# Optimization experiments

Measured on AMD Instinct MI355X. Metric: run time of the kernel, lower is better.

The kernel has to match this reference:

```python
import jax, jax.numpy as jnp
import numpy as np

EMBED = 768
HEADS = 12
HEAD_DIM = EMBED // HEADS
HIDDEN = 4 * EMBED
B, N = 8, 1024
EPS = 1e-5


def layernorm(x, g, b):
    mu = jnp.mean(x, axis=-1, keepdims=True)
    var = jnp.var(x, axis=-1, keepdims=True)
    return (x - mu) * jax.lax.rsqrt(var + EPS) * g + b


def setup_inputs() -> dict:
    key = jax.random.key(0)
    ks = jax.random.split(key, 8)
    s_qkv = 1.0 / np.sqrt(EMBED)
    s_fc1 = 1.0 / np.sqrt(EMBED)
    s_fc2 = 1.0 / np.sqrt(HIDDEN)
    return {
        "x": jax.random.normal(ks[0], (B, N, EMBED), dtype=jnp.float32),
        "ln1_g": jnp.ones((EMBED,), jnp.float32),
        "ln1_b": jnp.zeros((EMBED,), jnp.float32),
        "qkv_w": jax.random.uniform(ks[1], (3 * EMBED, EMBED), jnp.float32, -s_qkv, s_qkv),
        "qkv_b": jnp.zeros((3 * EMBED,), jnp.float32),
        "proj_w": jax.random.uniform(ks[2], (EMBED, EMBED), jnp.float32, -s_qkv, s_qkv),
        "proj_b": jnp.zeros((EMBED,), jnp.float32),
        "ln2_g": jnp.ones((EMBED,), jnp.float32),
        "ln2_b": jnp.zeros((EMBED,), jnp.float32),
        "fc1_w": jax.random.uniform(ks[3], (HIDDEN, EMBED), jnp.float32, -s_fc1, s_fc1),
        "fc1_b": jnp.zeros((HIDDEN,), jnp.float32),
        "fc2_w": jax.random.uniform(ks[4], (EMBED, HIDDEN), jnp.float32, -s_fc2, s_fc2),
        "fc2_b": jnp.zeros((EMBED,), jnp.float32),
    }


def reference(x, ln1_g, ln1_b, qkv_w, qkv_b, proj_w, proj_b,
              ln2_g, ln2_b, fc1_w, fc1_b, fc2_w, fc2_b):
    b, n, d = x.shape
    # --- attention sublayer ---
    h = layernorm(x, ln1_g, ln1_b)
    qkv = h @ qkv_w.T + qkv_b                      # [b,n,3d]
    qkv = qkv.reshape(b, n, 3, HEADS, HEAD_DIM).transpose(2, 0, 3, 1, 4)
    q, k, v = qkv[0], qkv[1], qkv[2]               # [b,h,n,hd]
    scores = jnp.einsum('bhqd,bhkd->bhqk', q, k) * (HEAD_DIM ** -0.5)
    attn = jax.nn.softmax(scores, axis=-1)
    ctx = jnp.einsum('bhqk,bhkd->bhqd', attn, v)   # [b,h,n,hd]
    ctx = ctx.transpose(0, 2, 1, 3).reshape(b, n, d)
    x = x + (ctx @ proj_w.T + proj_b)
    # --- MLP sublayer ---
    h = layernorm(x, ln2_g, ln2_b)
    h = jax.nn.gelu(h @ fc1_w.T + fc1_b, approximate=False)
    x = x + (h @ fc2_w.T + fc2_b)
    return x
```

## Files before the change

kernel.cpp:

```cpp
#include <hip/hip_runtime.h>
#include <cstdint>

typedef __bf16 bf16_t;
typedef __attribute__((ext_vector_type(8))) __bf16 bf16x8;
typedef __attribute__((ext_vector_type(4))) __bf16 bf16x4;
typedef __attribute__((ext_vector_type(4))) float f32x4;

#define MFMA16(a, b, c) __builtin_amdgcn_mfma_f32_16x16x32_bf16((a), (b), (c), 0, 0, 0)

#define GLOAD16(g, l) __builtin_amdgcn_global_load_lds(                      \
    (const __attribute__((address_space(1))) void*)(g),                      \
    (__attribute__((address_space(3))) void*)(l), 16, 0, 0)

__device__ inline float gelu_f(float v) {
    const float u = v + 0.044715f * v * v * v;
    return v / (1.0f + exp2f(-2.3022038f * u));
}

__global__ __launch_bounds__(256) void cvt4_kernel(const float* __restrict__ s0, bf16_t* __restrict__ d0,
                                                   const float* __restrict__ s1, bf16_t* __restrict__ d1,
                                                   const float* __restrict__ s2, bf16_t* __restrict__ d2,
                                                   const float* __restrict__ s3, bf16_t* __restrict__ d3) {
    const int blk = blockIdx.x;
    const float* s; bf16_t* d; int base;
    if (blk < 864)       { s = s0; d = d0; base = blk; }
    else if (blk < 1152) { s = s1; d = d1; base = blk - 864; }
    else if (blk < 2304) { s = s2; d = d2; base = blk - 1152; }
    else                 { s = s3; d = d3; base = blk - 2304; }
    const int i = (base * 256 + threadIdx.x) * 8;
    const float4* sp = (const float4*)(s + i);
    float4 a = sp[0], b = sp[1];
    bf16x8 o;
    o[0] = (bf16_t)a.x; o[1] = (bf16_t)a.y; o[2] = (bf16_t)a.z; o[3] = (bf16_t)a.w;
    o[4] = (bf16_t)b.x; o[5] = (bf16_t)b.y; o[6] = (bf16_t)b.z; o[7] = (bf16_t)b.w;
    *(bf16x8*)(d + i) = o;
}

__global__ __launch_bounds__(256) void ln_kernel(const float* __restrict__ x,
                                                 const float* __restrict__ gw,
                                                 const float* __restrict__ bw,
                                                 bf16_t* __restrict__ out) {
    const int row  = blockIdx.x * 4 + (threadIdx.x >> 6);
    const int lane = threadIdx.x & 63;
    const float4* xr = (const float4*)(x + (long)row * 768);
    float4 v[3];
    float s = 0.f, q = 0.f;
#pragma unroll
    for (int j = 0; j < 3; ++j) {
        v[j] = xr[j * 64 + lane];
        s += v[j].x + v[j].y + v[j].z + v[j].w;
        q += v[j].x * v[j].x + v[j].y * v[j].y + v[j].z * v[j].z + v[j].w * v[j].w;
    }
#pragma unroll
    for (int off = 32; off > 0; off >>= 1) {
        s += __shfl_xor(s, off);
        q += __shfl_xor(q, off);
    }
    const float mu = s * (1.0f / 768.0f);
    const float rs = rsqrtf(q * (1.0f / 768.0f) - mu * mu + 1e-5f);
#pragma unroll
    for (int j = 0; j < 3; ++j) {
        float4 g4 = ((const float4*)gw)[j * 64 + lane];
        float4 b4 = ((const float4*)bw)[j * 64 + lane];
        bf16x4 o;
        o[0] = (bf16_t)((v[j].x - mu) * rs * g4.x + b4.x);
        o[1] = (bf16_t)((v[j].y - mu) * rs * g4.y + b4.y);
        o[2] = (bf16_t)((v[j].z - mu) * rs * g4.z + b4.z);
        o[3] = (bf16_t)((v[j].w - mu) * rs * g4.w + b4.w);
        *(bf16x4*)(out + (long)row * 768 + (j * 64 + lane) * 4) = o;
    }
}

template <int MODE, int NC, int RPX>
__global__ __launch_bounds__(256) void gemm_bt(const bf16_t* __restrict__ A,
                                               const bf16_t* __restrict__ Bw,
                                               const float* __restrict__ bias,
                                               bf16_t* __restrict__ outb,
                                               bf16_t* __restrict__ o1,
                                               bf16_t* __restrict__ o2,
                                               int Nn, int K) {
    __shared__ __align__(16) bf16_t As[2][128 * 32];
    __shared__ __align__(16) bf16_t Bs[2][128 * 32];
    __shared__ __align__(16) bf16_t Ts[4 * 16 * 72];
    const int id = blockIdx.x;
    const int xcd = id & 7, sblk = id >> 3;
    const int tn = (sblk % NC) * 128;
    const int tm = (xcd * RPX + sblk / NC) * 128;
    const int w = threadIdx.x >> 6, l = threadIdx.x & 63;
    const int quad = l >> 4, r16 = l & 15;
    const int wm = (w >> 1) * 64, wn = (w & 1) * 64;
    f32x4 acc[4][4] = {};
    const bf16_t* ga = A  + (long)(tm + w * 32 + (l >> 2)) * K + (l & 3) * 8;
    const bf16_t* gb = Bw + (long)(tn + w * 32 + (l >> 2)) * K + (l & 3) * 8;
    const int lw = w * 1024;

    GLOAD16(ga,          &As[0][lw]);
    GLOAD16(ga + 16 * K, &As[0][lw + 512]);
    GLOAD16(gb,          &Bs[0][lw]);
    GLOAD16(gb + 16 * K, &Bs[0][lw + 512]);

    int cur = 0;
    for (int k0 = 0; k0 < K; k0 += 32) {
        asm volatile("s_waitcnt vmcnt(0)" ::: "memory");
        __syncthreads();
        if (k0 + 32 < K) {
            const bf16_t* gan = ga + k0 + 32;
            const bf16_t* gbn = gb + k0 + 32;
            GLOAD16(gan,          &As[cur ^ 1][lw]);
            GLOAD16(gan + 16 * K, &As[cur ^ 1][lw + 512]);
            GLOAD16(gbn,          &Bs[cur ^ 1][lw]);
            GLOAD16(gbn + 16 * K, &Bs[cur ^ 1][lw + 512]);
        }
        bf16x8 af[4], bfr[4];
#pragma unroll
        for (int i = 0; i < 4; ++i) {
            af[i]  = *(const bf16x8*)&As[cur][(wm + i * 16 + r16) * 32 + quad * 8];
            bfr[i] = *(const bf16x8*)&Bs[cur][(wn + i * 16 + r16) * 32 + quad * 8];
        }
#pragma unroll
        for (int i = 0; i < 4; ++i)
#pragma unroll
            for (int j = 0; j < 4; ++j)
                acc[i][j] = MFMA16(af[i], bfr[j], acc[i][j]);
        cur ^= 1;
    }

    bf16_t* tw = Ts + w * 16 * 72;
    if (MODE == 0) {
        const int sect = (tn + wn) / 768;
        const int cwb  = tn + wn - sect * 768;
        const int h    = cwb >> 6;
        if (sect == 2) {
#pragma unroll
            for (int i = 0; i < 4; ++i) {
                const int r0 = tm + wm + i * 16 + quad * 4;
                const int b = r0 >> 10, n0 = r0 & 1023;
#pragma unroll
                for (int j = 0; j < 4; ++j) {
                    const int d = j * 16 + r16;
                    const float bv = bias[tn + wn + j * 16 + r16];
                    bf16_t* dst = o2 + ((long)(b * 12 + h) * 64 + d) * 1024;
#pragma unroll
                    for (int rr = 0; rr < 4; ++rr) {
                        const int nn = n0 + rr;
                        const int c = ((nn & 15) << 3) | ((nn >> 4) & 7);
                        dst[(nn & 0x380) + c] = (bf16_t)(acc[i][j][rr] + bv);
                    }
                }
            }
        } else {
            bf16_t* dstbuf = (sect == 0 ? outb : o1);
#pragma unroll
            for (int i = 0; i < 4; ++i) {
#pragma unroll
                for (int j = 0; j < 4; ++j) {
                    const float bv = bias[tn + wn + j * 16 + r16];
#pragma unroll
                    for (int rr = 0; rr < 4; ++rr)
                        tw[(quad * 4 + rr) * 72 + j * 16 + r16] = (bf16_t)(acc[i][j][rr] + bv);
                }
                const int tok = tm + wm + i * 16 + (l >> 2);
                const int b = tok >> 10, n0 = tok & 1023;
                const long base = (long)(b * 12 + h) * 65536 + (long)n0 * 64;
#pragma unroll
                for (int it = 0; it < 2; ++it) {
                    bf16x8 vv = *(const bf16x8*)&tw[(l >> 2) * 72 + (l & 3) * 8 + it * 32];
                    *(bf16x8*)(dstbuf + base + (l & 3) * 8 + it * 32) = vv;
                }
            }
        }
    } else {
#pragma unroll
        for (int i = 0; i < 4; ++i) {
#pragma unroll
            for (int j = 0; j < 4; ++j) {
                const float bv = bias[tn + wn + j * 16 + r16];
#pragma unroll
                for (int rr = 0; rr < 4; ++rr)
                    tw[(quad * 4 + rr) * 72 + j * 16 + r16] = (bf16_t)gelu_f(acc[i][j][rr] + bv);
            }
            const int grow = tm + wm + i * 16 + (l >> 2);
#pragma unroll
            for (int it = 0; it < 2; ++it) {
                bf16x8 vv = *(const bf16x8*)&tw[(l >> 2) * 72 + (l & 3) * 8 + it * 32];
                *(bf16x8*)(outb + (long)grow * Nn + tn + wn + (l & 3) * 8 + it * 32) = vv;
            }
        }
    }
}

__global__ __launch_bounds__(256) void gemm_res64(const bf16_t* __restrict__ A,
                                                  const bf16_t* __restrict__ Bw,
                                                  const float* __restrict__ bias,
                                                  const float* __restrict__ res,
                                                  float* __restrict__ outf,
                                                  int Nn, int K) {
    __shared__ __align__(16) bf16_t As[2][64 * 32];
    __shared__ __align__(16) bf16_t Bs[2][128 * 32];
    __shared__ __align__(16) float  Tf[4 * 16 * 68];
    const int id = blockIdx.x;
    const int xcd = id & 7, sblk = id >> 3;
    const int tn = (sblk % 6) * 128;
    const int tm = (xcd * 16 + sblk / 6) * 64;
    const int w = threadIdx.x >> 6, l = threadIdx.x & 63;
    const int quad = l >> 4, r16 = l & 15;
    const int wm = (w >> 1) * 32, wn = (w & 1) * 64;
    f32x4 acc[2][4] = {};
    const bf16_t* ga = A  + (long)(tm + w * 16 + (l >> 2)) * K + (l & 3) * 8;
    const bf16_t* gb = Bw + (long)(tn + w * 32 + (l >> 2)) * K + (l & 3) * 8;
    const int lwa = w * 512, lwb = w * 1024;

    GLOAD16(ga,          &As[0][lwa]);
    GLOAD16(gb,          &Bs[0][lwb]);
    GLOAD16(gb + 16 * K, &Bs[0][lwb + 512]);

    int cur = 0;
    for (int k0 = 0; k0 < K; k0 += 32) {
        asm volatile("s_waitcnt vmcnt(0)" ::: "memory");
        __syncthreads();
        if (k0 + 32 < K) {
            const bf16_t* gan = ga + k0 + 32;
            const bf16_t* gbn = gb + k0 + 32;
            GLOAD16(gan,          &As[cur ^ 1][lwa]);
            GLOAD16(gbn,          &Bs[cur ^ 1][lwb]);
            GLOAD16(gbn + 16 * K, &Bs[cur ^ 1][lwb + 512]);
        }
        bf16x8 af[2], bfr[4];
#pragma unroll
        for (int i = 0; i < 2; ++i)
            af[i]  = *(const bf16x8*)&As[cur][(wm + i * 16 + r16) * 32 + quad * 8];
#pragma unroll
        for (int j = 0; j < 4; ++j)
            bfr[j] = *(const bf16x8*)&Bs[cur][(wn + j * 16 + r16) * 32 + quad * 8];
#pragma unroll
        for (int i = 0; i < 2; ++i)
#pragma unroll
            for (int j = 0; j < 4; ++j)
                acc[i][j] = MFMA16(af[i], bfr[j], acc[i][j]);
        cur ^= 1;
    }
    float* tf = Tf + w * 16 * 68;
#pragma unroll
    for (int i = 0; i < 2; ++i) {
#pragma unroll
        for (int j = 0; j < 4; ++j) {
            const float bv = bias[tn + wn + j * 16 + r16];
#pragma unroll
            for (int rr = 0; rr < 4; ++rr)
                tf[(quad * 4 + rr) * 68 + j * 16 + r16] = acc[i][j][rr] + bv;
        }
        const int grow = tm + wm + i * 16 + (l >> 2);
#pragma unroll
        for (int it = 0; it < 4; ++it) {
            const int gcol = tn + wn + (l & 3) * 4 + it * 16;
            f32x4 vv = *(const f32x4*)&tf[(l >> 2) * 68 + (l & 3) * 4 + it * 16];
            const float4 rv = *(const float4*)(res + (long)grow * Nn + gcol);
            float4 ov;
            ov.x = rv.x + vv[0]; ov.y = rv.y + vv[1];
            ov.z = rv.z + vv[2]; ov.w = rv.w + vv[3];
            *(float4*)(outf + (long)grow * Nn + gcol) = ov;
        }
    }
}

__global__ __launch_bounds__(256, 3) void attn_kernel(const bf16_t* __restrict__ qh,
                                                      const bf16_t* __restrict__ kh,
                                                      const bf16_t* __restrict__ vt,
                                                      bf16_t* __restrict__ ctx) {
    __shared__ __align__(16) bf16_t Ks[128 * 72];
    __shared__ __align__(16) bf16_t Vt[64 * 136];
    __shared__ __align__(16) bf16_t Ps[4 * 16 * 136];
    const int w = threadIdx.x >> 6, l = threadIdx.x & 63;
    const int quad = l >> 4, r16 = l & 15;
    const int bh = blockIdx.x, qt = blockIdx.y;
    const bf16_t* qp = qh + (long)bh * 65536;
    const bf16_t* kp = kh + (long)bh * 65536;
    const bf16_t* vp = vt + (long)bh * 65536;
    const int q0 = qt * 128 + w * 32;
    const float SC = 0.18033688011f;

    bf16x8 qf[2][2];
#pragma unroll
    for (int mt = 0; mt < 2; ++mt)
#pragma unroll
        for (int kq = 0; kq < 2; ++kq)
            qf[mt][kq] = *(const bf16x8*)(qp + (long)(q0 + mt * 16 + r16) * 64 + kq * 32 + quad * 8);

    float lsum[2][4] = {};
    f32x4 oacc[2][4] = {};
    bf16_t* pw = Ps + w * 16 * 136;

    bf16x8 kpre[4], vpre[4];
#pragma unroll
    for (int c = 0; c < 4; ++c) {
        const int cc = threadIdx.x + c * 256;
        kpre[c] = *(const bf16x8*)(kp + (long)(cc >> 3) * 64 + (cc & 7) * 8);
        vpre[c] = *(const bf16x8*)(vp + (long)(cc >> 4) * 1024 + (cc & 15) * 8);
    }

    for (int kt = 0; kt < 8; ++kt) {
        __syncthreads();
#pragma unroll
        for (int c = 0; c < 4; ++c) {
            const int cc = threadIdx.x + c * 256;
            *(bf16x8*)&Ks[(cc >> 3) * 72 + (cc & 7) * 8] = kpre[c];
            *(bf16x8*)&Vt[(cc >> 4) * 136 + (cc & 15) * 8] = vpre[c];
        }
        __syncthreads();
        if (kt < 7) {
            const int kb = (kt + 1) * 128;
#pragma unroll
            for (int c = 0; c < 4; ++c) {
                const int cc = threadIdx.x + c * 256;
                kpre[c] = *(const bf16x8*)(kp + (long)(kb + (cc >> 3)) * 64 + (cc & 7) * 8);
                vpre[c] = *(const bf16x8*)(vp + (long)(cc >> 4) * 1024 + kb + (cc & 15) * 8);
            }
        }

#pragma unroll
        for (int mt = 0; mt < 2; ++mt) {
            f32x4 s[8] = {};
#pragma unroll
            for (int nt = 0; nt < 8; ++nt) {
                bf16x8 kf0 = *(const bf16x8*)&Ks[(nt * 16 + r16) * 72 + quad * 8];
                bf16x8 kf1 = *(const bf16x8*)&Ks[(nt * 16 + r16) * 72 + 32 + quad * 8];
                s[nt] = MFMA16(qf[mt][0], kf0, s[nt]);
                s[nt] = MFMA16(qf[mt][1], kf1, s[nt]);
            }
#pragma unroll
            for (int rr = 0; rr < 4; ++rr) {
                bf16x8 pv;
#pragma unroll
                for (int nt = 0; nt < 8; ++nt) {
                    const float p = exp2f(s[nt][rr] * SC);
                    lsum[mt][rr] += p;
                    pv[nt] = (bf16_t)p;
                }
                *(bf16x8*)&pw[(quad * 4 + rr) * 136 + r16 * 8] = pv;
            }
#pragma unroll
            for (int kc = 0; kc < 4; ++kc) {
                bf16x8 pf = *(const bf16x8*)&pw[r16 * 136 + kc * 32 + quad * 8];
#pragma unroll
                for (int dt = 0; dt < 4; ++dt) {
                    bf16x8 vf = *(const bf16x8*)&Vt[(dt * 16 + r16) * 136 + kc * 32 + quad * 8];
                    oacc[mt][dt] = MFMA16(pf, vf, oacc[mt][dt]);
                }
            }
        }
    }
#pragma unroll
    for (int mt = 0; mt < 2; ++mt)
#pragma unroll
        for (int rr = 0; rr < 4; ++rr) {
#pragma unroll
            for (int off = 1; off < 16; off <<= 1)
                lsum[mt][rr] += __shfl_xor(lsum[mt][rr], off);
        }
    const int b = bh / 12, h = bh % 12;
    const long tb = (long)b * 1024;
#pragma unroll
    for (int mt = 0; mt < 2; ++mt) {
#pragma unroll
        for (int dt = 0; dt < 4; ++dt)
#pragma unroll
            for (int rr = 0; rr < 4; ++rr)
                pw[(quad * 4 + rr) * 72 + dt * 16 + r16] =
                    (bf16_t)(oacc[mt][dt][rr] / lsum[mt][rr]);
        const int tok = q0 + mt * 16 + (l >> 2);
        const int off = (l & 3) * 16;
        bf16_t* dst = ctx + (tb + tok) * 768 + h * 64 + off;
        const bf16_t* src = &pw[(l >> 2) * 72 + off];
#pragma unroll
        for (int it = 0; it < 2; ++it)
            *(bf16x8*)(dst + it * 8) = *(const bf16x8*)(src + it * 8);
    }
}

extern "C" void kernel_launch(void* const* d_in, const int* in_sizes, int n_in,
                              void* d_out, int out_size, void* d_ws, size_t ws_size,
                              hipStream_t stream) {
    const float* x      = (const float*)d_in[0];
    const float* ln1_g  = (const float*)d_in[1];
    const float* ln1_b  = (const float*)d_in[2];
    const float* qkv_w  = (const float*)d_in[3];
    const float* qkv_b  = (const float*)d_in[4];
    const float* proj_w = (const float*)d_in[5];
    const float* proj_b = (const float*)d_in[6];
    const float* ln2_g  = (const float*)d_in[7];
    const float* ln2_b  = (const float*)d_in[8];
    const float* fc1_w  = (const float*)d_in[9];
    const float* fc1_b  = (const float*)d_in[10];
    const float* fc2_w  = (const float*)d_in[11];
    const float* fc2_b  = (const float*)d_in[12];

    char* p = (char*)d_ws;
    bf16_t* wqkv  = (bf16_t*)p; p += (size_t)2304 * 768 * 2;
    bf16_t* wproj = (bf16_t*)p; p += (size_t)768 * 768 * 2;
    bf16_t* wfc1  = (bf16_t*)p; p += (size_t)3072 * 768 * 2;
    bf16_t* wfc2  = (bf16_t*)p; p += (size_t)768 * 3072 * 2;
    bf16_t* h1    = (bf16_t*)p; p += (size_t)8192 * 768 * 2;
    bf16_t* qhb   = (bf16_t*)p; p += (size_t)96 * 1024 * 64 * 2;
    bf16_t* khb   = (bf16_t*)p; p += (size_t)96 * 1024 * 64 * 2;
    bf16_t* vtb   = (bf16_t*)p; p += (size_t)96 * 64 * 1024 * 2;
    bf16_t* ctx   = (bf16_t*)p; p += (size_t)8192 * 768 * 2;
    float*  x2    = (float*)p;  p += (size_t)8192 * 768 * 4;
    bf16_t* h2    = (bf16_t*)p; p += (size_t)8192 * 768 * 2;
    bf16_t* a1    = (bf16_t*)p; p += (size_t)8192 * 3072 * 2;

    cvt4_kernel<<<3456, 256, 0, stream>>>(qkv_w, wqkv, proj_w, wproj, fc1_w, wfc1, fc2_w, wfc2);

    ln_kernel<<<2048, 256, 0, stream>>>(x, ln1_g, ln1_b, h1);
    gemm_bt<0, 18, 8><<<1152, 256, 0, stream>>>(h1, wqkv, qkv_b, qhb, khb, vtb, 2304, 768);
    attn_kernel<<<dim3(96, 8), 256, 0, stream>>>(qhb, khb, vtb, ctx);
    gemm_res64<<<768, 256, 0, stream>>>(ctx, wproj, proj_b, x, x2, 768, 768);
    ln_kernel<<<2048, 256, 0, stream>>>(x2, ln2_g, ln2_b, h2);
    gemm_bt<2, 24, 8><<<1536, 256, 0, stream>>>(h2, wfc1, fc1_b, a1, nullptr, nullptr, 3072, 768);
    gemm_res64<<<768, 256, 0, stream>>>(a1, wfc2, fc2_b, x2, (float*)d_out, 768, 3072);
}
```

Before: 379.4 us.

## Deepen GEMM global-to-LDS prefetch to triple and quad buffering

The two GEMM kernels move from a double-buffered K loop with a full vmcnt(0) wait per step to a 3-stage (gemm_bt) and 4-stage (gemm_res64) ring of LDS buffers. Partial vmcnt waits and a bare s_barrier keep two or three tiles of global-to-LDS loads in flight while MFMAs run. The epilogue staging buffers now alias the main LDS buffer behind a __syncthreads, which limits the growth in LDS footprint. The cost is more LDS per block, which may lower occupancy, plus extra barriers in the epilogue.

```diff
diff --git a/kernel.cpp b/kernel.cpp
--- a/kernel.cpp
+++ b/kernel.cpp
@@ -79,9 +79,9 @@
                                                bf16_t* __restrict__ o1,
                                                bf16_t* __restrict__ o2,
                                                int Nn, int K) {
-    __shared__ __align__(16) bf16_t As[2][128 * 32];
-    __shared__ __align__(16) bf16_t Bs[2][128 * 32];
-    __shared__ __align__(16) bf16_t Ts[4 * 16 * 72];
+    __shared__ __align__(16) char smem[3 * (128 * 32 + 128 * 32) * 2];
+    bf16_t* As = (bf16_t*)smem;
+    bf16_t* Bs = (bf16_t*)(smem + 3 * 128 * 32 * 2);
     const int id = blockIdx.x;
     const int xcd = id & 7, sblk = id >> 3;
     const int tn = (sblk % NC) * 128;
@@ -93,39 +93,48 @@
     const bf16_t* ga = A  + (long)(tm + w * 32 + (l >> 2)) * K + (l & 3) * 8;
     const bf16_t* gb = Bw + (long)(tn + w * 32 + (l >> 2)) * K + (l & 3) * 8;
     const int lw = w * 1024;
-
-    GLOAD16(ga,          &As[0][lw]);
-    GLOAD16(ga + 16 * K, &As[0][lw + 512]);
-    GLOAD16(gb,          &Bs[0][lw]);
-    GLOAD16(gb + 16 * K, &Bs[0][lw + 512]);
-
-    int cur = 0;
-    for (int k0 = 0; k0 < K; k0 += 32) {
-        asm volatile("s_waitcnt vmcnt(0)" ::: "memory");
-        __syncthreads();
-        if (k0 + 32 < K) {
-            const bf16_t* gan = ga + k0 + 32;
-            const bf16_t* gbn = gb + k0 + 32;
-            GLOAD16(gan,          &As[cur ^ 1][lw]);
-            GLOAD16(gan + 16 * K, &As[cur ^ 1][lw + 512]);
-            GLOAD16(gbn,          &Bs[cur ^ 1][lw]);
-            GLOAD16(gbn + 16 * K, &Bs[cur ^ 1][lw + 512]);
-        }
+    const int NK = K >> 5;
+
+    auto issue = [&](int t) {
+        const bf16_t* gan = ga + t * 32;
+        const bf16_t* gbn = gb + t * 32;
+        bf16_t* ab = As + (t % 3) * 4096;
+        bf16_t* bb = Bs + (t % 3) * 4096;
+        GLOAD16(gan,          ab + lw);
+        GLOAD16(gan + 16 * K, ab + lw + 512);
+        GLOAD16(gbn,          bb + lw);
+        GLOAD16(gbn + 16 * K, bb + lw + 512);
+    };
+    auto compute = [&](int t) {
+        const bf16_t* ab = As + (t % 3) * 4096;
+        const bf16_t* bb = Bs + (t % 3) * 4096;
         bf16x8 af[4], bfr[4];
 #pragma unroll
         for (int i = 0; i < 4; ++i) {
-            af[i]  = *(const bf16x8*)&As[cur][(wm + i * 16 + r16) * 32 + quad * 8];
-            bfr[i] = *(const bf16x8*)&Bs[cur][(wn + i * 16 + r16) * 32 + quad * 8];
+            af[i]  = *(const bf16x8*)&ab[(wm + i * 16 + r16) * 32 + quad * 8];
+            bfr[i] = *(const bf16x8*)&bb[(wn + i * 16 + r16) * 32 + quad * 8];
         }
 #pragma unroll
         for (int i = 0; i < 4; ++i)
 #pragma unroll
             for (int j = 0; j < 4; ++j)
                 acc[i][j] = MFMA16(af[i], bfr[j], acc[i][j]);
-        cur ^= 1;
-    }
-
-    bf16_t* tw = Ts + w * 16 * 72;
+    };
+
+    issue(0);
+    issue(1);
+    for (int t = 0; t < NK - 1; ++t) {
+        asm volatile("s_waitcnt vmcnt(4)" ::: "memory");
+        __builtin_amdgcn_s_barrier();
+        if (t + 2 < NK) issue(t + 2);
+        compute(t);
+    }
+    asm volatile("s_waitcnt vmcnt(0)" ::: "memory");
+    __builtin_amdgcn_s_barrier();
+    compute(NK - 1);
+
+    __syncthreads();
+    bf16_t* tw = (bf16_t*)smem + w * 16 * 72;
     if (MODE == 0) {
         const int sect = (tn + wn) / 768;
         const int cwb  = tn + wn - sect * 768;
@@ -195,9 +204,9 @@
                                                   const float* __restrict__ res,
                                                   float* __restrict__ outf,
                                                   int Nn, int K) {
-    __shared__ __align__(16) bf16_t As[2][64 * 32];
-    __shared__ __align__(16) bf16_t Bs[2][128 * 32];
-    __shared__ __align__(16) float  Tf[4 * 16 * 68];
+    __shared__ __align__(16) char smem[4 * (64 * 32 + 128 * 32) * 2];
+    bf16_t* As = (bf16_t*)smem;
+    bf16_t* Bs = (bf16_t*)(smem + 4 * 64 * 32 * 2);
     const int id = blockIdx.x;
     const int xcd = id & 7, sblk = id >> 3;
     const int tn = (sblk % 6) * 128;
@@ -209,37 +218,52 @@
     const bf16_t* ga = A  + (long)(tm + w * 16 + (l >> 2)) * K + (l & 3) * 8;
     const bf16_t* gb = Bw + (long)(tn + w * 32 + (l >> 2)) * K + (l & 3) * 8;
     const int lwa = w * 512, lwb = w * 1024;
-
-    GLOAD16(ga,          &As[0][lwa]);
-    GLOAD16(gb,          &Bs[0][lwb]);
-    GLOAD16(gb + 16 * K, &Bs[0][lwb + 512]);
-
-    int cur = 0;
-    for (int k0 = 0; k0 < K; k0 += 32) {
-        asm volatile("s_waitcnt vmcnt(0)" ::: "memory");
-        __syncthreads();
-        if (k0 + 32 < K) {
-            const bf16_t* gan = ga + k0 + 32;
-            const bf16_t* gbn = gb + k0 + 32;
-            GLOAD16(gan,          &As[cur ^ 1][lwa]);
-            GLOAD16(gbn,          &Bs[cur ^ 1][lwb]);
-            GLOAD16(gbn + 16 * K, &Bs[cur ^ 1][lwb + 512]);
-        }
+    const int NK = K >> 5;
+
+    auto issue = [&](int t) {
+        const bf16_t* gan = ga + t * 32;
+        const bf16_t* gbn = gb + t * 32;
+        bf16_t* ab = As + (t & 3) * 2048;
+        bf16_t* bb = Bs + (t & 3) * 4096;
+        GLOAD16(gan,          ab + lwa);
+        GLOAD16(gbn,          bb + lwb);
+        GLOAD16(gbn + 16 * K, bb + lwb + 512);
+    };
+    auto compute = [&](int t) {
+        const bf16_t* ab = As + (t & 3) * 2048;
+        const bf16_t* bb = Bs + (t & 3) * 4096;
         bf16x8 af[2], bfr[4];
 #pragma unroll
         for (int i = 0; i < 2; ++i)
-            af[i]  = *(const bf16x8*)&As[cur][(wm + i * 16 + r16) * 32 + quad * 8];
+            af[i]  = *(const bf16x8*)&ab[(wm + i * 16 + r16) * 32 + quad * 8];
 #pragma unroll
         for (int j = 0; j < 4; ++j)
-            bfr[j] = *(const bf16x8*)&Bs[cur][(wn + j * 16 + r16) * 32 + quad * 8];
+            bfr[j] = *(const bf16x8*)&bb[(wn + j * 16 + r16) * 32 + quad * 8];
 #pragma unroll
         for (int i = 0; i < 2; ++i)
 #pragma unroll
             for (int j = 0; j < 4; ++j)
                 acc[i][j] = MFMA16(af[i], bfr[j], acc[i][j]);
-        cur ^= 1;
-    }
-    float* tf = Tf + w * 16 * 68;
+    };
+
+    issue(0);
+    issue(1);
+    issue(2);
+    for (int t = 0; t < NK - 2; ++t) {
+        asm volatile("s_waitcnt vmcnt(6)" ::: "memory");
+        __builtin_amdgcn_s_barrier();
+        if (t + 3 < NK) issue(t + 3);
+        compute(t);
+    }
+    asm volatile("s_waitcnt vmcnt(3)" ::: "memory");
+    __builtin_amdgcn_s_barrier();
+    compute(NK - 2);
+    asm volatile("s_waitcnt vmcnt(0)" ::: "memory");
+    __builtin_amdgcn_s_barrier();
+    compute(NK - 1);
+
+    __syncthreads();
+    float* tf = (float*)smem + w * 16 * 68;
 #pragma unroll
     for (int i = 0; i < 2; ++i) {
 #pragma unroll
@@ -260,6 +284,7 @@
             ov.z = rv.z + vv[2]; ov.w = rv.w + vv[3];
             *(float4*)(outf + (long)grow * Nn + gcol) = ov;
         }
+        __syncthreads();
     }
 }
 
```

After: 360.9 us. 4.9% less time.
